# Kernel optimization log

Measured on AMD Instinct MI355X. Metric: run time of the kernel, lower is better.

The kernel has to match this reference:

```python
import jax, jax.numpy as jnp
import numpy as np

THRESH = 0.9
MIN_KEPT = 131072
IGNORE = -1


def setup_inputs() -> dict:
    key = jax.random.key(0)
    k1, k2, k3 = jax.random.split(key, 3)
    predict = jax.random.normal(k1, (8, 19, 768, 768), dtype=jnp.float32)
    target = jax.random.randint(k2, (8, 768, 768), 0, 19, dtype=jnp.int32)
    weight = jax.random.uniform(k3, (19,), dtype=jnp.float32) + 0.5
    return {"predict": predict, "target": target, "weight": weight}


def reference(predict, target, weight):
    # predict: (n, c, h, w); target: (n, h, w); weight: (c,)
    logp = jax.nn.log_softmax(predict, axis=1)              # (n, c, h, w)
    tmp_target = jnp.where(target == IGNORE, 0, target)     # ignore -> class 0 for gather
    # gather log-prob of the target class
    logp_t = jnp.take_along_axis(logp, tmp_target[:, None].astype(jnp.int32), axis=1)[:, 0]  # (n, h, w)
    prob = jnp.exp(logp_t)                                  # softmax prob at target class

    mask = (target != IGNORE).reshape(-1)                   # valid-pixel mask
    prob_flat = prob.reshape(-1)
    # push ignored pixels to +inf so they land at the end of the sort
    prob_valid = jnp.where(mask, prob_flat, jnp.inf)
    sorted_prob = jnp.sort(prob_valid)
    n_valid = jnp.sum(mask.astype(jnp.int32))
    kth = jnp.minimum(jnp.int32(MIN_KEPT), n_valid - 1)     # min(min_kept, numel-1)
    min_threshold = jnp.take(sorted_prob, kth)
    threshold = jnp.maximum(min_threshold, jnp.float32(THRESH))

    # per-pixel weighted CE, 0 on ignored pixels (matches torch ignore_index, reduction='none')
    loss = -jnp.take(weight, tmp_target) * logp_t           # (n, h, w)
    loss_flat = loss.reshape(-1)

    select = mask & (prob_flat < threshold)
    sel_f = select.astype(loss_flat.dtype)
    # 'elementwise_mean' over selected losses
    return jnp.sum(loss_flat * sel_f) / jnp.sum(sel_f)
```

## Files before the change

kernel.cpp:

```cpp
#include <hip/hip_runtime.h>
#include <stdint.h>

#define NCLS 19
#define HW   (768 * 768)
#define NPIX (8 * HW)
#define NGRP (NPIX / 4)
#define MINKEPT 131072u
#define NBINS 8192
#define BLOCK 256
#define GRID_MAIN (NGRP / BLOCK)

#define OFF_PSUM  ((size_t)0)
#define OFF_PCS   ((size_t)GRID_MAIN * 4)
#define OFF_PCV   ((size_t)GRID_MAIN * 8)
#define OFF_STATE ((size_t)GRID_MAIN * 12)
#define OFF_PROB  (OFF_STATE + 256)
#define OFF_LOSS  (OFF_PROB + (size_t)NPIX * 4)
#define OFF_HIST  (OFF_LOSS + (size_t)NPIX * 4)

typedef float    f4 __attribute__((ext_vector_type(4)));
typedef int      i4 __attribute__((ext_vector_type(4)));
typedef unsigned u4 __attribute__((ext_vector_type(4)));

struct Grp { u4 pb; f4 lo; float ls; unsigned sc; unsigned vc; };

__device__ __forceinline__ Grp compute4(const float* __restrict__ predict,
                                        const int* __restrict__ target,
                                        const float* __restrict__ wsh, int g)
{
    int n = g / HW;
    int p = g - n * HW;
    const float* base = predict + (size_t)n * ((size_t)NCLS * HW) + p;

    i4 t4 = __builtin_nontemporal_load((const i4*)(target + g));
    int tcx = (t4.x == -1) ? 0 : t4.x;
    int tcy = (t4.y == -1) ? 0 : t4.y;
    int tcz = (t4.z == -1) ? 0 : t4.z;
    int tcw = (t4.w == -1) ? 0 : t4.w;

    f4 s  = {0.f, 0.f, 0.f, 0.f};
    f4 vt = {0.f, 0.f, 0.f, 0.f};
#pragma unroll
    for (int c = 0; c < NCLS; ++c) {
        f4 v = __builtin_nontemporal_load((const f4*)(base + (size_t)c * HW));
        s.x += __expf(v.x); s.y += __expf(v.y);
        s.z += __expf(v.z); s.w += __expf(v.w);
        vt.x = (c == tcx) ? v.x : vt.x;
        vt.y = (c == tcy) ? v.y : vt.y;
        vt.z = (c == tcz) ? v.z : vt.z;
        vt.w = (c == tcw) ? v.w : vt.w;
    }

    bool vx = (t4.x != -1), vy = (t4.y != -1), vz = (t4.z != -1), vw = (t4.w != -1);
    float lpx = vt.x - __logf(s.x), lpy = vt.y - __logf(s.y);
    float lpz = vt.z - __logf(s.z), lpw = vt.w - __logf(s.w);
    float px = __expf(lpx), py = __expf(lpy), pz = __expf(lpz), pw = __expf(lpw);

    Grp r;
    r.pb.x = vx ? __float_as_uint(px) : 0x7F800000u;
    r.pb.y = vy ? __float_as_uint(py) : 0x7F800000u;
    r.pb.z = vz ? __float_as_uint(pz) : 0x7F800000u;
    r.pb.w = vw ? __float_as_uint(pw) : 0x7F800000u;
    r.lo.x = vx ? (-wsh[tcx] * lpx) : 0.f;
    r.lo.y = vy ? (-wsh[tcy] * lpy) : 0.f;
    r.lo.z = vz ? (-wsh[tcz] * lpz) : 0.f;
    r.lo.w = vw ? (-wsh[tcw] * lpw) : 0.f;
    bool sx = vx && (px < 0.9f), sy = vy && (py < 0.9f);
    bool sz = vz && (pz < 0.9f), sw = vw && (pw < 0.9f);
    r.ls = (sx ? r.lo.x : 0.f) + (sy ? r.lo.y : 0.f) +
           (sz ? r.lo.z : 0.f) + (sw ? r.lo.w : 0.f);
    r.sc = (unsigned)sx + (unsigned)sy + (unsigned)sz + (unsigned)sw;
    r.vc = (unsigned)vx + (unsigned)vy + (unsigned)vz + (unsigned)vw;
    return r;
}

__global__ __launch_bounds__(BLOCK) void k_main(
    const float* __restrict__ predict, const int* __restrict__ target,
    const float* __restrict__ weight, float* __restrict__ psum,
    unsigned* __restrict__ pcs, unsigned* __restrict__ pcv)
{
    __shared__ float wsh[32];
    __shared__ float red_f[4];
    __shared__ unsigned red_a[4], red_b[4];
    int tid = threadIdx.x, bid = blockIdx.x;
    if (tid < NCLS) wsh[tid] = weight[tid];
    __syncthreads();

    Grp r = compute4(predict, target, wsh, (bid * BLOCK + tid) * 4);
    float lsum = r.ls; unsigned scnt = r.sc, vcnt = r.vc;
#pragma unroll
    for (int d = 32; d > 0; d >>= 1) {
        lsum += __shfl_down(lsum, d);
        scnt += __shfl_down(scnt, d);
        vcnt += __shfl_down(vcnt, d);
    }
    if ((tid & 63) == 0) { red_f[tid >> 6] = lsum; red_a[tid >> 6] = scnt; red_b[tid >> 6] = vcnt; }
    __syncthreads();
    if (tid == 0) {
        psum[bid] = red_f[0] + red_f[1] + red_f[2] + red_f[3];
        pcs[bid]  = red_a[0] + red_a[1] + red_a[2] + red_a[3];
        pcv[bid]  = red_b[0] + red_b[1] + red_b[2] + red_b[3];
    }
}

__global__ __launch_bounds__(BLOCK) void k_decide(
    const float* __restrict__ psum, const unsigned* __restrict__ pcs,
    const unsigned* __restrict__ pcv, unsigned* __restrict__ state,
    float* __restrict__ out)
{
    __shared__ double red_d[4];
    __shared__ unsigned red_a[4], red_b[4];
    int tid = threadIdx.x;
    double ds = 0.0; unsigned cs = 0, cv = 0;
    for (int i = tid; i < GRID_MAIN; i += BLOCK) {
        ds += (double)psum[i]; cs += pcs[i]; cv += pcv[i];
    }
#pragma unroll
    for (int d = 32; d > 0; d >>= 1) {
        ds += __shfl_down(ds, d); cs += __shfl_down(cs, d); cv += __shfl_down(cv, d);
    }
    if ((tid & 63) == 0) { red_d[tid >> 6] = ds; red_a[tid >> 6] = cs; red_b[tid >> 6] = cv; }
    __syncthreads();
    if (tid == 0) {
        double sum = red_d[0] + red_d[1] + red_d[2] + red_d[3];
        unsigned cb = red_a[0] + red_a[1] + red_a[2] + red_a[3];
        unsigned nv = red_b[0] + red_b[1] + red_b[2] + red_b[3];
        unsigned km = nv - 1u;
        unsigned k  = (MINKEPT < km) ? MINKEPT : km;
        bool common = cb > k;
        state[4] = common ? 1u : 0u;
        state[5] = k;
        state[6] = 0u; state[7] = 0u; state[8] = 0u; state[9] = 0u;
        if (common) out[0] = (float)(sum / (double)cb);
    }
}

__global__ __launch_bounds__(BLOCK) void k_mat(
    const float* __restrict__ predict, const int* __restrict__ target,
    const float* __restrict__ weight, const unsigned* __restrict__ state,
    unsigned* __restrict__ probbits, float* __restrict__ lossbuf,
    unsigned* __restrict__ hist)
{
    if (state[4]) return;
    __shared__ float wsh[32];
    if (threadIdx.x < NCLS) wsh[threadIdx.x] = weight[threadIdx.x];
    __syncthreads();
    int stride = gridDim.x * BLOCK;
    for (int idx = blockIdx.x * BLOCK + threadIdx.x; idx < NGRP; idx += stride) {
        int g = idx * 4;
        Grp r = compute4(predict, target, wsh, g);
        *(u4*)(probbits + g) = r.pb;
        *(f4*)(lossbuf + g) = r.lo;
    }
    for (int i = blockIdx.x * BLOCK + threadIdx.x; i < NBINS; i += stride) hist[i] = 0;
}

__global__ __launch_bounds__(BLOCK) void k_hist_scan(
    const unsigned* __restrict__ probbits, unsigned* __restrict__ hist,
    unsigned* __restrict__ state, int level)
{
    if (state[4]) return;
    __shared__ unsigned h[NBINS];
    __shared__ unsigned wtot[4], wpre[4];
    __shared__ unsigned isLast;
    int tid = threadIdx.x;
    for (int i = tid; i < NBINS; i += BLOCK) h[i] = 0;
    __syncthreads();
    unsigned pref = (level == 0) ? 0u : state[0];
    int stride = gridDim.x * BLOCK;
    for (int i = blockIdx.x * BLOCK + tid; i < NPIX; i += stride) {
        unsigned pb = probbits[i];
        if (level == 0) atomicAdd(&h[pb >> 19], 1u);
        else if (level == 1) { if ((pb >> 19) == pref) atomicAdd(&h[(pb >> 6) & (NBINS - 1)], 1u); }
        else                 { if ((pb >> 6)  == pref) atomicAdd(&h[pb & 63u], 1u); }
    }
    __syncthreads();
    for (int i = tid; i < NBINS; i += BLOCK) {
        unsigned c = h[i];
        if (c) atomicAdd(&hist[i], c);
    }
    __threadfence();
    if (tid == 0) {
        unsigned old = __hip_atomic_fetch_add(&state[6 + level], 1u,
                                              __ATOMIC_ACQ_REL, __HIP_MEMORY_SCOPE_AGENT);
        isLast = (old == (unsigned)gridDim.x - 1u) ? 1u : 0u;
    }
    __syncthreads();
    if (!isLast) return;
    __threadfence();

    unsigned vals[32];
    unsigned s = 0;
#pragma unroll
    for (int j = 0; j < 32; ++j) {
        unsigned v = __hip_atomic_load(&hist[tid * 32 + j],
                                       __ATOMIC_RELAXED, __HIP_MEMORY_SCOPE_AGENT);
        vals[j] = v; s += v;
    }
    unsigned x = s;
    int lane = tid & 63, wid = tid >> 6;
    for (int d = 1; d < 64; d <<= 1) {
        unsigned y = __shfl_up(x, d);
        if (lane >= d) x += y;
    }
    if (lane == 63) wtot[wid] = x;
    __syncthreads();
    if (tid == 0) {
        unsigned a = 0;
        for (int i = 0; i < 4; ++i) { wpre[i] = a; a += wtot[i]; }
    }
    __syncthreads();
    unsigned excl = x + wpre[wid] - s;

    unsigned k = (level == 0) ? state[5] : state[1];

    if (s > 0 && k >= excl && k < excl + s) {
        unsigned rem = k - excl;
        unsigned cum = 0, kn = 0; int bsel = 0; bool found = false;
#pragma unroll
        for (int j = 0; j < 32; ++j) {
            if (!found && rem < cum + vals[j]) { bsel = j; kn = rem - cum; found = true; }
            cum += vals[j];
        }
        unsigned bin = (unsigned)(tid * 32 + bsel);
        if (level == 0)      { state[0] = bin;                state[1] = kn; }
        else if (level == 1) { state[0] = (pref << 13) | bin; state[1] = kn; }
        else {
            unsigned tb = (pref << 6) | bin;
            state[2] = __float_as_uint(fmaxf(__uint_as_float(tb), 0.9f));
        }
    }
    __syncthreads();
    for (int i = tid; i < NBINS; i += BLOCK) hist[i] = 0;
}

__global__ __launch_bounds__(BLOCK) void k_reduce_final(
    const unsigned* __restrict__ probbits, const float* __restrict__ lossbuf,
    unsigned* __restrict__ state, float* __restrict__ psum,
    unsigned* __restrict__ pcs, float* __restrict__ out)
{
    if (state[4]) return;
    unsigned tb = state[2];
    float s = 0.f; unsigned c = 0;
    int tid = threadIdx.x;
    int stride = gridDim.x * BLOCK;
    for (int i = blockIdx.x * BLOCK + tid; i < NPIX; i += stride) {
        unsigned pb = probbits[i];
        float l = lossbuf[i];
        if (pb < tb) { s += l; c++; }
    }
#pragma unroll
    for (int d = 32; d > 0; d >>= 1) { s += __shfl_down(s, d); c += __shfl_down(c, d); }
    __shared__ float sd[4];
    __shared__ unsigned cd[4];
    __shared__ unsigned isLast;
    int lane = tid & 63, wid = tid >> 6;
    if (lane == 0) { sd[wid] = s; cd[wid] = c; }
    __syncthreads();
    if (tid == 0) {
        psum[blockIdx.x] = sd[0] + sd[1] + sd[2] + sd[3];
        pcs[blockIdx.x]  = cd[0] + cd[1] + cd[2] + cd[3];
    }
    __threadfence();
    if (tid == 0) {
        unsigned old = __hip_atomic_fetch_add(&state[9], 1u,
                                              __ATOMIC_ACQ_REL, __HIP_MEMORY_SCOPE_AGENT);
        isLast = (old == (unsigned)gridDim.x - 1u) ? 1u : 0u;
    }
    __syncthreads();
    if (!isLast) return;
    __threadfence();

    double ds = 0.0; unsigned ct = 0;
    for (int i = tid; i < (int)gridDim.x; i += BLOCK) {
        float pv; unsigned cvv;
        pv  = __hip_atomic_load(&psum[i], __ATOMIC_RELAXED, __HIP_MEMORY_SCOPE_AGENT);
        cvv = __hip_atomic_load(&pcs[i],  __ATOMIC_RELAXED, __HIP_MEMORY_SCOPE_AGENT);
        ds += (double)pv; ct += cvv;
    }
#pragma unroll
    for (int d = 32; d > 0; d >>= 1) { ds += __shfl_down(ds, d); ct += __shfl_down(ct, d); }
    __shared__ double rd[4];
    __shared__ unsigned ra[4];
    if (lane == 0) { rd[wid] = ds; ra[wid] = ct; }
    __syncthreads();
    if (tid == 0) {
        double dt = rd[0] + rd[1] + rd[2] + rd[3];
        unsigned cc = ra[0] + ra[1] + ra[2] + ra[3];
        out[0] = (float)(dt / (double)cc);
    }
}

extern "C" void kernel_launch(void* const* d_in, const int* in_sizes, int n_in,
                              void* d_out, int out_size, void* d_ws, size_t ws_size,
                              hipStream_t stream)
{
    const float* predict = (const float*)d_in[0];
    const int*   target  = (const int*)d_in[1];
    const float* weight  = (const float*)d_in[2];
    char* ws = (char*)d_ws;
    float* out = (float*)d_out;

    float*    psum     = (float*)(ws + OFF_PSUM);
    unsigned* pcs      = (unsigned*)(ws + OFF_PCS);
    unsigned* pcv      = (unsigned*)(ws + OFF_PCV);
    unsigned* state    = (unsigned*)(ws + OFF_STATE);
    unsigned* probbits = (unsigned*)(ws + OFF_PROB);
    float*    lossbuf  = (float*)(ws + OFF_LOSS);
    unsigned* hist     = (unsigned*)(ws + OFF_HIST);

    k_main<<<GRID_MAIN, BLOCK, 0, stream>>>(predict, target, weight, psum, pcs, pcv);
    k_decide<<<1, BLOCK, 0, stream>>>(psum, pcs, pcv, state, out);
    k_mat<<<1024, BLOCK, 0, stream>>>(predict, target, weight, state,
                                      probbits, lossbuf, hist);
    k_hist_scan<<<512, BLOCK, 0, stream>>>(probbits, hist, state, 0);
    k_hist_scan<<<512, BLOCK, 0, stream>>>(probbits, hist, state, 1);
    k_hist_scan<<<512, BLOCK, 0, stream>>>(probbits, hist, state, 2);
    k_reduce_final<<<512, BLOCK, 0, stream>>>(probbits, lossbuf, state, psum, pcs, out);
}
```

Baseline: 460.6 us.

## Fold fallback selection path into single-block decide kernel

Merges the decide, materialize, three histogram-scan levels and the final reduction into one single-block kernel, so the launch sequence shrinks from seven kernels to two. On the common path, where enough pixels fall below the fixed threshold, this removes the launch overhead of the early-returning kernels. The rare fallback path now runs on one block of 256 threads over all pixels, which would be very slow if it were ever taken.

Measured after the change: 452.5 us. About the same (-1.7%).

```diff
diff --git a/kernel.cpp b/kernel.cpp
--- a/kernel.cpp
+++ b/kernel.cpp
@@ -13,10 +13,8 @@
 #define OFF_PSUM  ((size_t)0)
 #define OFF_PCS   ((size_t)GRID_MAIN * 4)
 #define OFF_PCV   ((size_t)GRID_MAIN * 8)
-#define OFF_STATE ((size_t)GRID_MAIN * 12)
-#define OFF_PROB  (OFF_STATE + 256)
+#define OFF_PROB  ((size_t)GRID_MAIN * 12)
 #define OFF_LOSS  (OFF_PROB + (size_t)NPIX * 4)
-#define OFF_HIST  (OFF_LOSS + (size_t)NPIX * 4)
 
 typedef float    f4 __attribute__((ext_vector_type(4)));
 typedef int      i4 __attribute__((ext_vector_type(4)));
@@ -103,14 +101,25 @@
     }
 }
 
-__global__ __launch_bounds__(BLOCK) void k_decide(
+__global__ __launch_bounds__(BLOCK) void k_decide_fb(
+    const float* __restrict__ predict, const int* __restrict__ target,
+    const float* __restrict__ weight,
     const float* __restrict__ psum, const unsigned* __restrict__ pcs,
-    const unsigned* __restrict__ pcv, unsigned* __restrict__ state,
+    const unsigned* __restrict__ pcv,
+    unsigned* __restrict__ probbits, float* __restrict__ lossbuf,
     float* __restrict__ out)
 {
     __shared__ double red_d[4];
     __shared__ unsigned red_a[4], red_b[4];
+    __shared__ unsigned sh_common, sh_k;
+    __shared__ float wsh[32];
+    __shared__ unsigned h[NBINS];
+    __shared__ unsigned wtot[4], wpre[4];
+    __shared__ unsigned sel_bin, sel_rem;
+
     int tid = threadIdx.x;
+    int lane = tid & 63, wid = tid >> 6;
+
     double ds = 0.0; unsigned cs = 0, cv = 0;
     for (int i = tid; i < GRID_MAIN; i += BLOCK) {
         ds += (double)psum[i]; cs += pcs[i]; cv += pcv[i];
@@ -119,7 +128,7 @@
     for (int d = 32; d > 0; d >>= 1) {
         ds += __shfl_down(ds, d); cs += __shfl_down(cs, d); cv += __shfl_down(cv, d);
     }
-    if ((tid & 63) == 0) { red_d[tid >> 6] = ds; red_a[tid >> 6] = cs; red_b[tid >> 6] = cv; }
+    if (lane == 0) { red_d[wid] = ds; red_a[wid] = cs; red_b[wid] = cv; }
     __syncthreads();
     if (tid == 0) {
         double sum = red_d[0] + red_d[1] + red_d[2] + red_d[3];
@@ -128,165 +137,86 @@
         unsigned km = nv - 1u;
         unsigned k  = (MINKEPT < km) ? MINKEPT : km;
         bool common = cb > k;
-        state[4] = common ? 1u : 0u;
-        state[5] = k;
-        state[6] = 0u; state[7] = 0u; state[8] = 0u; state[9] = 0u;
+        sh_common = common ? 1u : 0u;
+        sh_k = k;
         if (common) out[0] = (float)(sum / (double)cb);
     }
-}
-
-__global__ __launch_bounds__(BLOCK) void k_mat(
-    const float* __restrict__ predict, const int* __restrict__ target,
-    const float* __restrict__ weight, const unsigned* __restrict__ state,
-    unsigned* __restrict__ probbits, float* __restrict__ lossbuf,
-    unsigned* __restrict__ hist)
-{
-    if (state[4]) return;
-    __shared__ float wsh[32];
-    if (threadIdx.x < NCLS) wsh[threadIdx.x] = weight[threadIdx.x];
-    __syncthreads();
-    int stride = gridDim.x * BLOCK;
-    for (int idx = blockIdx.x * BLOCK + threadIdx.x; idx < NGRP; idx += stride) {
+    __syncthreads();
+    if (sh_common) return;
+
+    unsigned k = sh_k;
+    if (tid < NCLS) wsh[tid] = weight[tid];
+    __syncthreads();
+
+    for (int idx = tid; idx < NGRP; idx += BLOCK) {
         int g = idx * 4;
         Grp r = compute4(predict, target, wsh, g);
         *(u4*)(probbits + g) = r.pb;
-        *(f4*)(lossbuf + g) = r.lo;
-    }
-    for (int i = blockIdx.x * BLOCK + threadIdx.x; i < NBINS; i += stride) hist[i] = 0;
-}
-
-__global__ __launch_bounds__(BLOCK) void k_hist_scan(
-    const unsigned* __restrict__ probbits, unsigned* __restrict__ hist,
-    unsigned* __restrict__ state, int level)
-{
-    if (state[4]) return;
-    __shared__ unsigned h[NBINS];
-    __shared__ unsigned wtot[4], wpre[4];
-    __shared__ unsigned isLast;
-    int tid = threadIdx.x;
-    for (int i = tid; i < NBINS; i += BLOCK) h[i] = 0;
-    __syncthreads();
-    unsigned pref = (level == 0) ? 0u : state[0];
-    int stride = gridDim.x * BLOCK;
-    for (int i = blockIdx.x * BLOCK + tid; i < NPIX; i += stride) {
+        *(f4*)(lossbuf + g)  = r.lo;
+    }
+    __syncthreads();
+
+    unsigned pref = 0, krem = k, tb = 0;
+    for (int level = 0; level < 3; ++level) {
+        for (int i = tid; i < NBINS; i += BLOCK) h[i] = 0;
+        __syncthreads();
+        for (int i = tid; i < NPIX; i += BLOCK) {
+            unsigned pb = probbits[i];
+            if (level == 0) atomicAdd(&h[pb >> 19], 1u);
+            else if (level == 1) { if ((pb >> 19) == pref) atomicAdd(&h[(pb >> 6) & (NBINS - 1)], 1u); }
+            else                 { if ((pb >> 6)  == pref) atomicAdd(&h[pb & 63u], 1u); }
+        }
+        __syncthreads();
+
+        unsigned vals[32];
+        unsigned s = 0;
+#pragma unroll
+        for (int j = 0; j < 32; ++j) { vals[j] = h[tid * 32 + j]; s += vals[j]; }
+        unsigned x = s;
+        for (int d = 1; d < 64; d <<= 1) {
+            unsigned y = __shfl_up(x, d);
+            if (lane >= d) x += y;
+        }
+        if (lane == 63) wtot[wid] = x;
+        __syncthreads();
+        if (tid == 0) {
+            unsigned a = 0;
+            for (int i = 0; i < 4; ++i) { wpre[i] = a; a += wtot[i]; }
+        }
+        __syncthreads();
+        unsigned excl = x + wpre[wid] - s;
+
+        if (s > 0 && krem >= excl && krem < excl + s) {
+            unsigned rem = krem - excl;
+            unsigned cum = 0, kn = 0; int bsel = 0; bool found = false;
+#pragma unroll
+            for (int j = 0; j < 32; ++j) {
+                if (!found && rem < cum + vals[j]) { bsel = j; kn = rem - cum; found = true; }
+                cum += vals[j];
+            }
+            sel_bin = (unsigned)(tid * 32 + bsel);
+            sel_rem = kn;
+        }
+        __syncthreads();
+        if (level == 0)      { pref = sel_bin;               krem = sel_rem; }
+        else if (level == 1) { pref = (pref << 13) | sel_bin; krem = sel_rem; }
+        else                 { tb = (pref << 6) | sel_bin; }
+        __syncthreads();
+    }
+
+    unsigned tbits = __float_as_uint(fmaxf(__uint_as_float(tb), 0.9f));
+    double sacc = 0.0; unsigned c = 0;
+    for (int i = tid; i < NPIX; i += BLOCK) {
         unsigned pb = probbits[i];
-        if (level == 0) atomicAdd(&h[pb >> 19], 1u);
-        else if (level == 1) { if ((pb >> 19) == pref) atomicAdd(&h[(pb >> 6) & (NBINS - 1)], 1u); }
-        else                 { if ((pb >> 6)  == pref) atomicAdd(&h[pb & 63u], 1u); }
-    }
-    __syncthreads();
-    for (int i = tid; i < NBINS; i += BLOCK) {
-        unsigned c = h[i];
-        if (c) atomicAdd(&hist[i], c);
-    }
-    __threadfence();
+        if (pb < tbits) { sacc += (double)lossbuf[i]; c++; }
+    }
+#pragma unroll
+    for (int d = 32; d > 0; d >>= 1) { sacc += __shfl_down(sacc, d); c += __shfl_down(c, d); }
+    if (lane == 0) { red_d[wid] = sacc; red_a[wid] = c; }
+    __syncthreads();
     if (tid == 0) {
-        unsigned old = __hip_atomic_fetch_add(&state[6 + level], 1u,
-                                              __ATOMIC_ACQ_REL, __HIP_MEMORY_SCOPE_AGENT);
-        isLast = (old == (unsigned)gridDim.x - 1u) ? 1u : 0u;
-    }
-    __syncthreads();
-    if (!isLast) return;
-    __threadfence();
-
-    unsigned vals[32];
-    unsigned s = 0;
-#pragma unroll
-    for (int j = 0; j < 32; ++j) {
-        unsigned v = __hip_atomic_load(&hist[tid * 32 + j],
-                                       __ATOMIC_RELAXED, __HIP_MEMORY_SCOPE_AGENT);
-        vals[j] = v; s += v;
-    }
-    unsigned x = s;
-    int lane = tid & 63, wid = tid >> 6;
-    for (int d = 1; d < 64; d <<= 1) {
-        unsigned y = __shfl_up(x, d);
-        if (lane >= d) x += y;
-    }
-    if (lane == 63) wtot[wid] = x;
-    __syncthreads();
-    if (tid == 0) {
-        unsigned a = 0;
-        for (int i = 0; i < 4; ++i) { wpre[i] = a; a += wtot[i]; }
-    }
-    __syncthreads();
-    unsigned excl = x + wpre[wid] - s;
-
-    unsigned k = (level == 0) ? state[5] : state[1];
-
-    if (s > 0 && k >= excl && k < excl + s) {
-        unsigned rem = k - excl;
-        unsigned cum = 0, kn = 0; int bsel = 0; bool found = false;
-#pragma unroll
-        for (int j = 0; j < 32; ++j) {
-            if (!found && rem < cum + vals[j]) { bsel = j; kn = rem - cum; found = true; }
-            cum += vals[j];
-        }
-        unsigned bin = (unsigned)(tid * 32 + bsel);
-        if (level == 0)      { state[0] = bin;                state[1] = kn; }
-        else if (level == 1) { state[0] = (pref << 13) | bin; state[1] = kn; }
-        else {
-            unsigned tb = (pref << 6) | bin;
-            state[2] = __float_as_uint(fmaxf(__uint_as_float(tb), 0.9f));
-        }
-    }
-    __syncthreads();
-    for (int i = tid; i < NBINS; i += BLOCK) hist[i] = 0;
-}
-
-__global__ __launch_bounds__(BLOCK) void k_reduce_final(
-    const unsigned* __restrict__ probbits, const float* __restrict__ lossbuf,
-    unsigned* __restrict__ state, float* __restrict__ psum,
-    unsigned* __restrict__ pcs, float* __restrict__ out)
-{
-    if (state[4]) return;
-    unsigned tb = state[2];
-    float s = 0.f; unsigned c = 0;
-    int tid = threadIdx.x;
-    int stride = gridDim.x * BLOCK;
-    for (int i = blockIdx.x * BLOCK + tid; i < NPIX; i += stride) {
-        unsigned pb = probbits[i];
-        float l = lossbuf[i];
-        if (pb < tb) { s += l; c++; }
-    }
-#pragma unroll
-    for (int d = 32; d > 0; d >>= 1) { s += __shfl_down(s, d); c += __shfl_down(c, d); }
-    __shared__ float sd[4];
-    __shared__ unsigned cd[4];
-    __shared__ unsigned isLast;
-    int lane = tid & 63, wid = tid >> 6;
-    if (lane == 0) { sd[wid] = s; cd[wid] = c; }
-    __syncthreads();
-    if (tid == 0) {
-        psum[blockIdx.x] = sd[0] + sd[1] + sd[2] + sd[3];
-        pcs[blockIdx.x]  = cd[0] + cd[1] + cd[2] + cd[3];
-    }
-    __threadfence();
-    if (tid == 0) {
-        unsigned old = __hip_atomic_fetch_add(&state[9], 1u,
-                                              __ATOMIC_ACQ_REL, __HIP_MEMORY_SCOPE_AGENT);
-        isLast = (old == (unsigned)gridDim.x - 1u) ? 1u : 0u;
-    }
-    __syncthreads();
-    if (!isLast) return;
-    __threadfence();
-
-    double ds = 0.0; unsigned ct = 0;
-    for (int i = tid; i < (int)gridDim.x; i += BLOCK) {
-        float pv; unsigned cvv;
-        pv  = __hip_atomic_load(&psum[i], __ATOMIC_RELAXED, __HIP_MEMORY_SCOPE_AGENT);
-        cvv = __hip_atomic_load(&pcs[i],  __ATOMIC_RELAXED, __HIP_MEMORY_SCOPE_AGENT);
-        ds += (double)pv; ct += cvv;
-    }
-#pragma unroll
-    for (int d = 32; d > 0; d >>= 1) { ds += __shfl_down(ds, d); ct += __shfl_down(ct, d); }
-    __shared__ double rd[4];
-    __shared__ unsigned ra[4];
-    if (lane == 0) { rd[wid] = ds; ra[wid] = ct; }
-    __syncthreads();
-    if (tid == 0) {
-        double dt = rd[0] + rd[1] + rd[2] + rd[3];
-        unsigned cc = ra[0] + ra[1] + ra[2] + ra[3];
+        double dt = red_d[0] + red_d[1] + red_d[2] + red_d[3];
+        unsigned cc = red_a[0] + red_a[1] + red_a[2] + red_a[3];
         out[0] = (float)(dt / (double)cc);
     }
 }
@@ -304,17 +234,10 @@
     float*    psum     = (float*)(ws + OFF_PSUM);
     unsigned* pcs      = (unsigned*)(ws + OFF_PCS);
     unsigned* pcv      = (unsigned*)(ws + OFF_PCV);
-    unsigned* state    = (unsigned*)(ws + OFF_STATE);
     unsigned* probbits = (unsigned*)(ws + OFF_PROB);
     float*    lossbuf  = (float*)(ws + OFF_LOSS);
-    unsigned* hist     = (unsigned*)(ws + OFF_HIST);
 
     k_main<<<GRID_MAIN, BLOCK, 0, stream>>>(predict, target, weight, psum, pcs, pcv);
-    k_decide<<<1, BLOCK, 0, stream>>>(psum, pcs, pcv, state, out);
-    k_mat<<<1024, BLOCK, 0, stream>>>(predict, target, weight, state,
-                                      probbits, lossbuf, hist);
-    k_hist_scan<<<512, BLOCK, 0, stream>>>(probbits, hist, state, 0);
-    k_hist_scan<<<512, BLOCK, 0, stream>>>(probbits, hist, state, 1);
-    k_hist_scan<<<512, BLOCK, 0, stream>>>(probbits, hist, state, 2);
-    k_reduce_final<<<512, BLOCK, 0, stream>>>(probbits, lossbuf, state, psum, pcs, out);
-}
+    k_decide_fb<<<1, BLOCK, 0, stream>>>(predict, target, weight,
+                                         psum, pcs, pcv, probbits, lossbuf, out);
+}
```
